# Kernel tuning notes

Measured on AMD Instinct MI355X. Metric: run time of the kernel, lower is better.

Reference implementation:

```python
import jax, jax.numpy as jnp
import numpy as np

N_HEAD = 16
DROP_P = 0.1


def setup_inputs() -> dict:
    key = jax.random.key(0)
    ks = jax.random.split(key, 5)
    B, T, C = 2, 2048, 1024
    return {
        "x": jax.random.normal(ks[0], (B, T, C), dtype=jnp.float32),
        "w_attn": jax.random.normal(ks[1], (C, 3 * C), dtype=jnp.float32) * 0.02,
        "b_attn": jax.random.normal(ks[2], (3 * C,), dtype=jnp.float32) * 0.02,
        "w_proj": jax.random.normal(ks[3], (C, C), dtype=jnp.float32) * 0.02,
        "b_proj": jax.random.normal(ks[4], (C,), dtype=jnp.float32) * 0.02,
    }


def reference(x, w_attn, b_attn, w_proj, b_proj):
    B, T, C = x.shape
    H = N_HEAD
    D = C // H  # head dim
    qkv = x @ w_attn + b_attn                      # [B,T,3C]
    q, k, v = jnp.split(qkv, 3, axis=-1)
    # [B,T,C] -> [B,H,T,D]
    q = q.reshape(B, T, H, D).transpose(0, 2, 1, 3)
    k = k.reshape(B, T, H, D).transpose(0, 2, 1, 3)
    v = v.reshape(B, T, H, D).transpose(0, 2, 1, 3)
    scale = 1.0 / jnp.sqrt(jnp.float32(D))
    attn = jnp.einsum("bhqd,bhkd->bhqk", q, k) * scale  # [B,H,T,T]
    causal = jnp.tril(jnp.ones((T, T), dtype=bool))
    attn = jnp.where(causal[None, None], attn, jnp.float32(-jnp.inf))
    attn = jax.nn.softmax(attn, axis=-1)
    # dropout p=0.1 (training mode in original); deterministic fixed key here
    keep = jax.random.bernoulli(jax.random.key(42), 1.0 - DROP_P, attn.shape)
    attn = jnp.where(keep, attn / (1.0 - DROP_P), 0.0)
    out = jnp.einsum("bhqk,bhkd->bhqd", attn, v)   # [B,H,T,D]
    out = out.transpose(0, 2, 1, 3).reshape(B, T, C)
    return out @ w_proj + b_proj
```

## Files before the change

### kernel.cpp

```cpp
#include <hip/hip_runtime.h>
#include <hip/hip_bf16.h>
#include <stdint.h>
#include <math.h>

#define TSEQ   2048
#define NBATCH 2
#define NHEAD  16
#define HDIM   64
#define CDIM   1024

#define KEEP_LIMIT 3865470464u
#define QSC 0.18033688011112042f

typedef short  bf16x8 __attribute__((ext_vector_type(8)));
typedef float  f32x4  __attribute__((ext_vector_type(4)));

__device__ __forceinline__ float fast_exp2(float x) {
    float r; asm("v_exp_f32 %0, %1" : "=v"(r) : "v"(x)); return r;
}
__device__ __forceinline__ uint32_t cvt_pk_bf16(float a, float b) {
    uint32_t r; asm("v_cvt_pk_bf16_f32 %0, %1, %2" : "=v"(r) : "v"(a), "v"(b)); return r;
}

__device__ __forceinline__ uint32_t rotl32(uint32_t x, int r) {
    return __builtin_amdgcn_alignbit(x, x, 32 - r);
}

__device__ __forceinline__ uint32_t tf2x32_xor(uint32_t x0, uint32_t x1) {
    const uint32_t ka = 0u, kb = 42u;
    const uint32_t kc = ka ^ kb ^ 0x1BD11BDAu;
    x0 += ka; x1 += kb;
#define TFR(r) { x0 += x1; x1 = rotl32(x1, r); x1 ^= x0; }
    TFR(13) TFR(15) TFR(26) TFR(6)
    x0 += kb; x1 += kc + 1u;
    TFR(17) TFR(29) TFR(16) TFR(24)
    x0 += kc; x1 += ka + 2u;
    TFR(13) TFR(15) TFR(26) TFR(6)
    x0 += ka; x1 += kb + 3u;
    TFR(17) TFR(29) TFR(16) TFR(24)
    x0 += kb; x1 += kc + 4u;
    TFR(13) TFR(15) TFR(26) TFR(6)
    x0 += kc; x1 += ka + 5u;
#undef TFR
    return x0 ^ x1;
}

__device__ __forceinline__ float bf2f(ushort u) {
    union { uint32_t i; float f; } c; c.i = ((uint32_t)u) << 16; return c.f;
}

__device__ __forceinline__ void async_copy16(void* lds, const void* g) {
    __builtin_amdgcn_global_load_lds(
        (const __attribute__((address_space(1))) unsigned int*)g,
        (__attribute__((address_space(3))) unsigned int*)lds, 16, 0, 0);
}

__global__ __launch_bounds__(256) void gen_mask(unsigned long long* __restrict__ mask)
{
    const int lane = threadIdx.x & 63;
    const int wv   = threadIdx.x >> 6;
    const int pair = blockIdx.x;
    const int hb   = blockIdx.y;
    const int half = blockIdx.z;
    for (int pass = 0; pass < 2; ++pass) {
        const int qt = pass ? 31 - pair : pair;
        const int nk = qt + 1;
        const int h0 = half ? (nk + 1) >> 1 : 0;
        const int h1 = half ? nk : (nk + 1) >> 1;
        const int ntask = (h1 - h0) << 6;
        const uint32_t qbase = ((uint32_t)hb << 11) + (uint32_t)(qt << 6);
        for (int t = wv; t < ntask; t += 4) {
            const int q  = t & 63;
            const int kt = h0 + (t >> 6);
            const uint32_t idx = (qbase + (uint32_t)q) * 2048u + (uint32_t)(kt << 6) + (uint32_t)lane;
            const bool keep = tf2x32_xor(0u, idx) < KEEP_LIMIT;
            const unsigned long long bal = __ballot(keep);
            if (lane == 0)
                mask[((size_t)(qbase + (uint32_t)q) << 5) + kt] = bal;
        }
    }
}

__global__ __launch_bounds__(256) void cvt_bf16(
    const float* __restrict__ src, ushort* __restrict__ dst, int n)
{
    int idx = (blockIdx.x * 256 + threadIdx.x) * 8;
    if (idx >= n) return;
    float4 a = *(const float4*)(src + idx);
    float4 b = *(const float4*)(src + idx + 4);
    uint4 o;
    o.x = cvt_pk_bf16(a.x, a.y); o.y = cvt_pk_bf16(a.z, a.w);
    o.z = cvt_pk_bf16(b.x, b.y); o.w = cvt_pk_bf16(b.z, b.w);
    *(uint4*)(dst + idx) = o;
}

__global__ __launch_bounds__(256) void transpose_cvt(
    const float* __restrict__ src, ushort* __restrict__ dst, int K, int N)
{
    __shared__ float t[32][33];
    const int n0 = blockIdx.x * 32, k0 = blockIdx.y * 32;
    const int i = threadIdx.x;
    {
        int k = i >> 3, n4 = (i & 7) * 4;
        float4 v = *(const float4*)(src + (size_t)(k0 + k) * N + n0 + n4);
        t[k][n4 + 0] = v.x; t[k][n4 + 1] = v.y; t[k][n4 + 2] = v.z; t[k][n4 + 3] = v.w;
    }
    __syncthreads();
    {
        int n = i >> 3, k4 = (i & 7) * 4;
        uint2 o;
        o.x = cvt_pk_bf16(t[k4 + 0][n], t[k4 + 1][n]);
        o.y = cvt_pk_bf16(t[k4 + 2][n], t[k4 + 3][n]);
        *(uint2*)(dst + (size_t)(n0 + n) * K + k0 + k4) = o;
    }
}

template<int MODE>
__global__ __launch_bounds__(256) void gemm_bf16(
    const ushort* __restrict__ A, const ushort* __restrict__ Bt,
    const float* __restrict__ bias,
    ushort* __restrict__ Q, ushort* __restrict__ Kq, ushort* __restrict__ V,
    float* __restrict__ Cf, int M, int N, int K)
{
    __shared__ ushort As[2][128 * 32];
    __shared__ ushort Bs[2][128 * 32];
    const int tid = threadIdx.x, lane = tid & 63, wid = tid >> 6;
    const int l15 = lane & 15, l4 = lane >> 4;
    const int wr = wid >> 1, wc = wid & 1;
    const int bn = blockIdx.x, bm = blockIdx.y;
    const int NTK = K >> 5;

    f32x4 acc[4][4];
#pragma unroll
    for (int m = 0; m < 4; ++m)
#pragma unroll
        for (int n = 0; n < 4; ++n) acc[m][n] = (f32x4){0.f, 0.f, 0.f, 0.f};

    auto stage = [&](int p, int k0) {
#pragma unroll
        for (int j = 0; j < 2; ++j) {
            const int rbase = wid * 32 + j * 16;
            const int row = rbase + (lane >> 2);
            const ushort* src = A + (size_t)(bm * 128 + row) * K + k0 + (lane & 3) * 8;
            async_copy16(&As[p][rbase * 32], src);
        }
#pragma unroll
        for (int j = 0; j < 2; ++j) {
            const int rbase = wid * 32 + j * 16;
            const int row = rbase + (lane >> 2);
            const ushort* src = Bt + (size_t)(bn * 128 + row) * K + k0 + (lane & 3) * 8;
            async_copy16(&Bs[p][rbase * 32], src);
        }
    };
    auto compute = [&](int p) {
        bf16x8 af[4], bf[4];
#pragma unroll
        for (int m = 0; m < 4; ++m)
            af[m] = *(const bf16x8*)&As[p][(wr * 64 + m * 16 + l15) * 32 + l4 * 8];
#pragma unroll
        for (int n = 0; n < 4; ++n)
            bf[n] = *(const bf16x8*)&Bs[p][(wc * 64 + n * 16 + l15) * 32 + l4 * 8];
#pragma unroll
        for (int m = 0; m < 4; ++m)
#pragma unroll
            for (int n = 0; n < 4; ++n)
                acc[m][n] = __builtin_amdgcn_mfma_f32_16x16x32_bf16(af[m], bf[n], acc[m][n], 0, 0, 0);
    };

    stage(0, 0);
    __syncthreads();
    for (int t = 0; t < NTK; ++t) {
        const int p = t & 1;
        if (t + 1 < NTK) stage(p ^ 1, (t + 1) << 5);
        compute(p);
        __syncthreads();
    }

    const int colbase = bn * 128 + wc * 64;
    const int rowbase = bm * 128 + wr * 64;
    if (MODE == 0) {
#pragma unroll
        for (int n = 0; n < 4; ++n) {
            const int col = colbase + n * 16 + l15;
            const float bv = bias[col];
#pragma unroll
            for (int m = 0; m < 4; ++m)
#pragma unroll
                for (int r = 0; r < 4; ++r) {
                    const int row = rowbase + m * 16 + l4 * 4 + r;
                    Cf[(size_t)row * N + col] = acc[m][n][r] + bv;
                }
        }
    } else {
#pragma unroll
        for (int n = 0; n < 4; ++n) {
            const int col = colbase + n * 16 + l15;
            const int which = col >> 10, cc = col & 1023;
            const int hh = cc >> 6, dd = cc & 63;
            const float bv = bias[col];
            const float sc = (which == 0) ? QSC : 1.0f;
#pragma unroll
            for (int m = 0; m < 4; ++m) {
                float v0 = (acc[m][n][0] + bv) * sc, v1 = (acc[m][n][1] + bv) * sc;
                float v2 = (acc[m][n][2] + bv) * sc, v3 = (acc[m][n][3] + bv) * sc;
                uint32_t pk01 = cvt_pk_bf16(v0, v1), pk23 = cvt_pk_bf16(v2, v3);
                ushort vals[4] = { (ushort)pk01, (ushort)(pk01 >> 16),
                                   (ushort)pk23, (ushort)(pk23 >> 16) };
#pragma unroll
                for (int r = 0; r < 4; ++r) {
                    const int row = rowbase + m * 16 + l4 * 4 + r;
                    const int bb = row >> 11, tt = row & 2047;
                    if (which == 0)
                        Q[(((size_t)(bb * NHEAD + hh)) * TSEQ + tt) * HDIM + dd] = vals[r];
                    else if (which == 1)
                        Kq[(((size_t)(bb * NHEAD + hh)) * TSEQ + tt) * HDIM + dd] = vals[r];
                    else
                        V[(((size_t)(bb * NHEAD + hh)) * HDIM + dd) * TSEQ + tt] = vals[r];
                }
            }
        }
    }
}

__global__ __launch_bounds__(256) void attn_fwd_mfma(
    const ushort* __restrict__ Qb, const ushort* __restrict__ Kb,
    const ushort* __restrict__ VbT, const unsigned long long* __restrict__ Mk,
    ushort* __restrict__ Ap, float* __restrict__ lp)
{
    __shared__ ushort Ks[64 * 64];
    __shared__ ushort Vt[2][64 * 64];
    __shared__ ushort Ps[64 * 64];
    const int tid = threadIdx.x;
    const int lane = tid & 63;
    const int wid = tid >> 6;
    const int l15 = lane & 15, l4 = lane >> 4;
    const int pair = blockIdx.x >> 1, half = blockIdx.x & 1;
    const int h = blockIdx.y, b = blockIdx.z;
    const int hb = b * NHEAD + h;
    const size_t headoff = (size_t)hb * TSEQ * HDIM;
    const ushort* Qg = Qb + headoff;
    const ushort* Kg = Kb + headoff;
    const ushort* Vg = VbT + headoff;

    auto stageK = [&](int kt) {
        const ushort* Kt = Kg + (size_t)(kt * 64) * HDIM;
#pragma unroll
        for (int c = 0; c < 2; ++c) {
            const int rbase = wid * 16 + c * 8;
            const int row = rbase + (lane >> 3);
            const ushort* srcK = Kt + row * 64 + (((lane & 7) * 8) ^ ((row & 7) << 3));
            async_copy16(&Ks[rbase * 64], srcK);
        }
    };
    auto stageV = [&](int p, int kt) {
        const ushort* Vt0 = Vg + kt * 64;
#pragma unroll
        for (int c = 0; c < 2; ++c) {
            const int rbase = wid * 16 + c * 8;
            const int row = rbase + (lane >> 3);
            const ushort* srcV = Vt0 + (size_t)row * TSEQ + (((lane & 7) * 8) ^ ((row & 7) << 3));
            async_copy16(&Vt[p][rbase * 64], srcV);
        }
    };

    const int swq = (l15 & 7) << 3;
    const int prow = wid * 16 + l15;

    for (int pass = 0; pass < 2; ++pass) {
        const int qt = pass ? (TSEQ / 64 - 1) - pair : pair;
        const int ntk = qt + 1;
        const int kb = half ? (ntk + 1) >> 1 : 0;
        const int ke = half ? ntk : (ntk + 1) >> 1;
        const int pidx = (hb * 32 + qt) * 2 + half;
        const int tilerow = wid * 16 + l15;
        ushort* arow = Ap + (size_t)pidx * 4096 + tilerow * 64;

        if (kb >= ke) {
#pragma unroll
            for (int dt = 0; dt < 4; ++dt) {
                ushort4 z; z.x = z.y = z.z = z.w = 0;
                *(ushort4*)&arow[dt * 16 + l4 * 4] = z;
            }
            if (l4 == 0) lp[pidx * 64 + tilerow] = 0.f;
            continue;
        }

        const int qglob = qt * 64 + tilerow;
        const unsigned long long* mrow = Mk + ((size_t)(hb * TSEQ + qglob) << 5);
        bf16x8 qf0, qf1;
        {
            const ushort* qrow = Qg + (size_t)qglob * HDIM;
            qf0 = *(const bf16x8*)(qrow + l4 * 8);
            qf1 = *(const bf16x8*)(qrow + 32 + l4 * 8);
        }

        f32x4 oacc[4];
#pragma unroll
        for (int i = 0; i < 4; ++i) oacc[i] = (f32x4){0.f, 0.f, 0.f, 0.f};
        float li = 0.f;

        stageK(kb);
        stageV(0, kb);
        __syncthreads();

        for (int kt = kb; kt < ke; ++kt) {
            const int p = (kt - kb) & 1;
            const bool hasNext = (kt + 1 < ke);
            if (hasNext) stageV(p ^ 1, kt + 1);

            const unsigned long long m64 = mrow[kt];

            f32x4 s4[4];
#pragma unroll
            for (int ct = 0; ct < 4; ++ct) {
                const int krow = ct * 16 + l15;
                const int sw = (krow & 7) << 3;
                bf16x8 kf0 = *(const bf16x8*)&Ks[krow * 64 + ((l4 * 8) ^ sw)];
                bf16x8 kf1 = *(const bf16x8*)&Ks[krow * 64 + ((l4 * 8 + 32) ^ sw)];
                f32x4 a = {0.f, 0.f, 0.f, 0.f};
                a = __builtin_amdgcn_mfma_f32_16x16x32_bf16(kf0, qf0, a, 0, 0, 0);
                a = __builtin_amdgcn_mfma_f32_16x16x32_bf16(kf1, qf1, a, 0, 0, 0);
                s4[ct] = a;
            }
            __syncthreads();
            if (hasNext) stageK(kt + 1);

            const int kb0 = kt * 64;
            if (kt == qt) {
#pragma unroll
                for (int ct = 0; ct < 4; ++ct)
#pragma unroll
                    for (int r = 0; r < 4; ++r) {
                        const int kglob = kb0 + ct * 16 + l4 * 4 + r;
                        s4[ct][r] = (kglob <= qglob) ? s4[ct][r] : -INFINITY;
                    }
            }
            float rs = 0.f;
#pragma unroll
            for (int ct = 0; ct < 4; ++ct)
#pragma unroll
                for (int r = 0; r < 4; ++r) {
                    s4[ct][r] = fast_exp2(s4[ct][r]);
                    rs += s4[ct][r];
                }
            li += rs;

#pragma unroll
            for (int ct = 0; ct < 4; ++ct) {
                const uint32_t nib = (uint32_t)(m64 >> (ct * 16 + l4 * 4)) & 0xFu;
                const float p0 = (nib & 1u) ? s4[ct][0] : 0.f;
                const float p1 = (nib & 2u) ? s4[ct][1] : 0.f;
                const float p2 = (nib & 4u) ? s4[ct][2] : 0.f;
                const float p3 = (nib & 8u) ? s4[ct][3] : 0.f;
                uint2 pk;
                pk.x = cvt_pk_bf16(p0, p1);
                pk.y = cvt_pk_bf16(p2, p3);
                *(uint2*)&Ps[prow * 64 + ((ct * 16 + l4 * 4) ^ swq)] = pk;
            }

            bf16x8 pf0 = *(const bf16x8*)&Ps[prow * 64 + ((l4 * 8) ^ swq)];
            bf16x8 pf1 = *(const bf16x8*)&Ps[prow * 64 + ((l4 * 8 + 32) ^ swq)];
#pragma unroll
            for (int dt = 0; dt < 4; ++dt) {
                const int drow = dt * 16 + l15;
                const int swv = (drow & 7) << 3;
                bf16x8 vf0 = *(const bf16x8*)&Vt[p][drow * 64 + ((l4 * 8) ^ swv)];
                bf16x8 vf1 = *(const bf16x8*)&Vt[p][drow * 64 + ((l4 * 8 + 32) ^ swv)];
                oacc[dt] = __builtin_amdgcn_mfma_f32_16x16x32_bf16(vf0, pf0, oacc[dt], 0, 0, 0);
                oacc[dt] = __builtin_amdgcn_mfma_f32_16x16x32_bf16(vf1, pf1, oacc[dt], 0, 0, 0);
            }
            __syncthreads();
        }

#pragma unroll
        for (int dt = 0; dt < 4; ++dt) {
            uint2 o;
            o.x = cvt_pk_bf16(oacc[dt][0], oacc[dt][1]);
            o.y = cvt_pk_bf16(oacc[dt][2], oacc[dt][3]);
            *(uint2*)&arow[dt * 16 + l4 * 4] = o;
        }
        float rs = li;
        rs += __shfl_xor(rs, 16);
        rs += __shfl_xor(rs, 32);
        if (l4 == 0) lp[pidx * 64 + tilerow] = rs;
    }
}

__global__ __launch_bounds__(256) void attn_merge(
    const ushort* __restrict__ Ap, const float* __restrict__ lp,
    ushort* __restrict__ AO)
{
    const int gidx = blockIdx.x * 16 + (threadIdx.x >> 4);
    const int hb = gidx >> 11;
    const int q  = gidx & 2047;
    const int qt = q >> 6, row = q & 63;
    const int sub = (threadIdx.x & 15) * 4;
    const int pidx0 = (hb * 32 + qt) * 2;
    const int pr = pidx0 * 64 + row;
    const float l0 = lp[pr], l1 = lp[pr + 64];
    const float inv = 1.0f / ((l0 + l1) * 0.9f);
    ushort4 a0 = *(const ushort4*)&Ap[(size_t)pidx0 * 4096 + row * 64 + sub];
    ushort4 a1 = *(const ushort4*)&Ap[(size_t)(pidx0 + 1) * 4096 + row * 64 + sub];
    const int b = hb >> 4, h = hb & 15;
    ushort* orow = AO + ((size_t)(b * TSEQ + q)) * CDIM + h * HDIM + sub;
    uint2 o;
    o.x = cvt_pk_bf16((bf2f(a0.x) + bf2f(a1.x)) * inv,
                      (bf2f(a0.y) + bf2f(a1.y)) * inv);
    o.y = cvt_pk_bf16((bf2f(a0.z) + bf2f(a1.z)) * inv,
                      (bf2f(a0.w) + bf2f(a1.w)) * inv);
    *(uint2*)orow = o;
}

extern "C" void kernel_launch(void* const* d_in, const int* in_sizes, int n_in,
                              void* d_out, int out_size, void* d_ws, size_t ws_size,
                              hipStream_t stream)
{
    const float* x      = (const float*)d_in[0];
    const float* w_attn = (const float*)d_in[1];
    const float* b_attn = (const float*)d_in[2];
    const float* w_proj = (const float*)d_in[3];
    const float* b_proj = (const float*)d_in[4];
    float* out = (float*)d_out;

    const size_t NH = (size_t)NBATCH * NHEAD * TSEQ * HDIM;
    ushort* Qb  = (ushort*)d_ws;
    ushort* Kb  = Qb + NH;
    ushort* VbT = Kb + NH;
    ushort* AO  = VbT + NH;
    ushort* xb  = AO + NH;
    ushort* wTa = xb + NH;
    ushort* wTp = wTa + (size_t)3072 * 1024;
    unsigned long long* Mk = (unsigned long long*)(wTp + (size_t)1024 * 1024);
    float*  lp  = (float*)(Mk + (size_t)65536 * 32);

    ushort* Aparts = (ushort*)d_out;

    cvt_bf16<<<2048, 256, 0, stream>>>(x, xb, 4096 * 1024);
    transpose_cvt<<<dim3(96, 32), 256, 0, stream>>>(w_attn, wTa, 1024, 3072);
    transpose_cvt<<<dim3(32, 32), 256, 0, stream>>>(w_proj, wTp, 1024, 1024);

    gemm_bf16<1><<<dim3(24, 32), 256, 0, stream>>>(
        xb, wTa, b_attn, Qb, Kb, VbT, nullptr, 4096, 3072, 1024);

    gen_mask<<<dim3(16, 32, 2), 256, 0, stream>>>(Mk);

    attn_fwd_mfma<<<dim3(32, NHEAD, NBATCH), 256, 0, stream>>>(
        Qb, Kb, VbT, Mk, Aparts, lp);

    attn_merge<<<4096, 256, 0, stream>>>(Aparts, lp, AO);

    gemm_bf16<0><<<dim3(8, 32), 256, 0, stream>>>(
        AO, wTp, b_proj, nullptr, nullptr, nullptr, out, 4096, 1024, 1024);
}
```

Measured before the change: 278.6 us.

## Merge prep kernels and co-schedule dropout mask generation with QKV GEMM

Folds the x conversion and both weight transposes into one prep launch. Merges dropout mask generation into the QKV GEMM launch as extra blocks, so the threefry hashing runs on CUs left idle by the 768 GEMM tiles. The mask blocks also get a new work split with four hashes in flight per wave. This cuts launch overhead and overlaps ALU-bound mask work with the MFMA-bound GEMM, at the cost of a more complex dispatch with heterogeneous blocks in one grid.

New measurement: 268.8 us. 3.5% less time.

```diff
diff --git a/kernel.cpp b/kernel.cpp
--- a/kernel.cpp
+++ b/kernel.cpp
@@ -55,51 +55,32 @@
         (__attribute__((address_space(3))) unsigned int*)lds, 16, 0, 0);
 }
 
-__global__ __launch_bounds__(256) void gen_mask(unsigned long long* __restrict__ mask)
-{
-    const int lane = threadIdx.x & 63;
-    const int wv   = threadIdx.x >> 6;
-    const int pair = blockIdx.x;
-    const int hb   = blockIdx.y;
-    const int half = blockIdx.z;
-    for (int pass = 0; pass < 2; ++pass) {
-        const int qt = pass ? 31 - pair : pair;
-        const int nk = qt + 1;
-        const int h0 = half ? (nk + 1) >> 1 : 0;
-        const int h1 = half ? nk : (nk + 1) >> 1;
-        const int ntask = (h1 - h0) << 6;
-        const uint32_t qbase = ((uint32_t)hb << 11) + (uint32_t)(qt << 6);
-        for (int t = wv; t < ntask; t += 4) {
-            const int q  = t & 63;
-            const int kt = h0 + (t >> 6);
-            const uint32_t idx = (qbase + (uint32_t)q) * 2048u + (uint32_t)(kt << 6) + (uint32_t)lane;
-            const bool keep = tf2x32_xor(0u, idx) < KEEP_LIMIT;
-            const unsigned long long bal = __ballot(keep);
-            if (lane == 0)
-                mask[((size_t)(qbase + (uint32_t)q) << 5) + kt] = bal;
-        }
-    }
-}
-
-__global__ __launch_bounds__(256) void cvt_bf16(
-    const float* __restrict__ src, ushort* __restrict__ dst, int n)
-{
-    int idx = (blockIdx.x * 256 + threadIdx.x) * 8;
-    if (idx >= n) return;
-    float4 a = *(const float4*)(src + idx);
-    float4 b = *(const float4*)(src + idx + 4);
-    uint4 o;
-    o.x = cvt_pk_bf16(a.x, a.y); o.y = cvt_pk_bf16(a.z, a.w);
-    o.z = cvt_pk_bf16(b.x, b.y); o.w = cvt_pk_bf16(b.z, b.w);
-    *(uint4*)(dst + idx) = o;
-}
-
-__global__ __launch_bounds__(256) void transpose_cvt(
-    const float* __restrict__ src, ushort* __restrict__ dst, int K, int N)
+__global__ __launch_bounds__(256) void prep(
+    const float* __restrict__ x, ushort* __restrict__ xb,
+    const float* __restrict__ wA, ushort* __restrict__ wTa,
+    const float* __restrict__ wP, ushort* __restrict__ wTp)
 {
     __shared__ float t[32][33];
-    const int n0 = blockIdx.x * 32, k0 = blockIdx.y * 32;
+    const int nb = blockIdx.x;
     const int i = threadIdx.x;
+    if (nb < 2048) {
+        int idx = (nb * 256 + i) * 8;
+        float4 a = *(const float4*)(x + idx);
+        float4 b = *(const float4*)(x + idx + 4);
+        uint4 o;
+        o.x = cvt_pk_bf16(a.x, a.y); o.y = cvt_pk_bf16(a.z, a.w);
+        o.z = cvt_pk_bf16(b.x, b.y); o.w = cvt_pk_bf16(b.z, b.w);
+        *(uint4*)(xb + idx) = o;
+        return;
+    }
+    const float* src; ushort* dst; int n0, k0, N, K;
+    if (nb < 5120) {
+        int tt = nb - 2048;  src = wA; dst = wTa;
+        n0 = (tt % 96) * 32; k0 = (tt / 96) * 32; N = 3072; K = 1024;
+    } else {
+        int tt = nb - 5120;  src = wP; dst = wTp;
+        n0 = (tt & 31) * 32; k0 = (tt >> 5) * 32; N = 1024; K = 1024;
+    }
     {
         int k = i >> 3, n4 = (i & 7) * 4;
         float4 v = *(const float4*)(src + (size_t)(k0 + k) * N + n0 + n4);
@@ -115,12 +96,136 @@
     }
 }
 
-template<int MODE>
-__global__ __launch_bounds__(256) void gemm_bf16(
+__global__ __launch_bounds__(256) void qkv_mask(
     const ushort* __restrict__ A, const ushort* __restrict__ Bt,
     const float* __restrict__ bias,
     ushort* __restrict__ Q, ushort* __restrict__ Kq, ushort* __restrict__ V,
-    float* __restrict__ Cf, int M, int N, int K)
+    unsigned long long* __restrict__ mask)
+{
+    __shared__ ushort As[2][128 * 32];
+    __shared__ ushort Bs[2][128 * 32];
+    const int tid = threadIdx.x, lane = tid & 63, wid = tid >> 6;
+
+    if (blockIdx.x >= 768) {
+        const int mb   = blockIdx.x - 768;
+        const int hb   = mb >> 6;
+        const int rem  = mb & 63;
+        const int pair = rem >> 2;
+        const int quad = rem & 3;
+        const int lim  = (pair + 1) << 6;
+        const int base = quad * 528 + wid * 132;
+#pragma unroll 1
+        for (int it = 0; it < 33; ++it) {
+            uint32_t idxs[4], qrow[4]; int kts[4];
+#pragma unroll
+            for (int j = 0; j < 4; ++j) {
+                const int u = base + it * 4 + j;
+                const bool first = (u < lim);
+                const int qt = first ? pair : 31 - pair;
+                const int uu = first ? u : u - lim;
+                const int kt = uu >> 6, q = uu & 63;
+                qrow[j] = ((uint32_t)hb << 11) + (uint32_t)((qt << 6) + q);
+                idxs[j] = qrow[j] * 2048u + (uint32_t)(kt << 6) + (uint32_t)lane;
+                kts[j] = kt;
+            }
+            uint32_t bits[4];
+#pragma unroll
+            for (int j = 0; j < 4; ++j) bits[j] = tf2x32_xor(0u, idxs[j]);
+#pragma unroll
+            for (int j = 0; j < 4; ++j) {
+                const unsigned long long bal = __ballot(bits[j] < KEEP_LIMIT);
+                if (lane == j)
+                    mask[((size_t)qrow[j] << 5) + kts[j]] = bal;
+            }
+        }
+        return;
+    }
+
+    const int l15 = lane & 15, l4 = lane >> 4;
+    const int wr = wid >> 1, wc = wid & 1;
+    const int bn = blockIdx.x % 24, bm = blockIdx.x / 24;
+    const int K = 1024, NTK = K >> 5;
+
+    f32x4 acc[4][4];
+#pragma unroll
+    for (int m = 0; m < 4; ++m)
+#pragma unroll
+        for (int n = 0; n < 4; ++n) acc[m][n] = (f32x4){0.f, 0.f, 0.f, 0.f};
+
+    auto stage = [&](int p, int k0) {
+#pragma unroll
+        for (int j = 0; j < 2; ++j) {
+            const int rbase = wid * 32 + j * 16;
+            const int row = rbase + (lane >> 2);
+            const ushort* src = A + (size_t)(bm * 128 + row) * K + k0 + (lane & 3) * 8;
+            async_copy16(&As[p][rbase * 32], src);
+        }
+#pragma unroll
+        for (int j = 0; j < 2; ++j) {
+            const int rbase = wid * 32 + j * 16;
+            const int row = rbase + (lane >> 2);
+            const ushort* src = Bt + (size_t)(bn * 128 + row) * K + k0 + (lane & 3) * 8;
+            async_copy16(&Bs[p][rbase * 32], src);
+        }
+    };
+    auto compute = [&](int p) {
+        bf16x8 af[4], bf[4];
+#pragma unroll
+        for (int m = 0; m < 4; ++m)
+            af[m] = *(const bf16x8*)&As[p][(wr * 64 + m * 16 + l15) * 32 + l4 * 8];
+#pragma unroll
+        for (int n = 0; n < 4; ++n)
+            bf[n] = *(const bf16x8*)&Bs[p][(wc * 64 + n * 16 + l15) * 32 + l4 * 8];
+#pragma unroll
+        for (int m = 0; m < 4; ++m)
+#pragma unroll
+            for (int n = 0; n < 4; ++n)
+                acc[m][n] = __builtin_amdgcn_mfma_f32_16x16x32_bf16(af[m], bf[n], acc[m][n], 0, 0, 0);
+    };
+
+    stage(0, 0);
+    __syncthreads();
+    for (int t = 0; t < NTK; ++t) {
+        const int p = t & 1;
+        if (t + 1 < NTK) stage(p ^ 1, (t + 1) << 5);
+        compute(p);
+        __syncthreads();
+    }
+
+    const int colbase = bn * 128 + wc * 64;
+    const int rowbase = bm * 128 + wr * 64;
+#pragma unroll
+    for (int n = 0; n < 4; ++n) {
+        const int col = colbase + n * 16 + l15;
+        const int which = col >> 10, cc = col & 1023;
+        const int hh = cc >> 6, dd = cc & 63;
+        const float bv = bias[col];
+        const float sc = (which == 0) ? QSC : 1.0f;
+#pragma unroll
+        for (int m = 0; m < 4; ++m) {
+            float v0 = (acc[m][n][0] + bv) * sc, v1 = (acc[m][n][1] + bv) * sc;
+            float v2 = (acc[m][n][2] + bv) * sc, v3 = (acc[m][n][3] + bv) * sc;
+            uint32_t pk01 = cvt_pk_bf16(v0, v1), pk23 = cvt_pk_bf16(v2, v3);
+            ushort vals[4] = { (ushort)pk01, (ushort)(pk01 >> 16),
+                               (ushort)pk23, (ushort)(pk23 >> 16) };
+#pragma unroll
+            for (int r = 0; r < 4; ++r) {
+                const int row = rowbase + m * 16 + l4 * 4 + r;
+                const int bb = row >> 11, tt = row & 2047;
+                if (which == 0)
+                    Q[(((size_t)(bb * NHEAD + hh)) * TSEQ + tt) * HDIM + dd] = vals[r];
+                else if (which == 1)
+                    Kq[(((size_t)(bb * NHEAD + hh)) * TSEQ + tt) * HDIM + dd] = vals[r];
+                else
+                    V[(((size_t)(bb * NHEAD + hh)) * HDIM + dd) * TSEQ + tt] = vals[r];
+            }
+        }
+    }
+}
+
+__global__ __launch_bounds__(256) void proj_gemm(
+    const ushort* __restrict__ A, const ushort* __restrict__ Bt,
+    const float* __restrict__ bias, float* __restrict__ Cf, int M, int N, int K)
 {
     __shared__ ushort As[2][128 * 32];
     __shared__ ushort Bs[2][128 * 32];
@@ -178,47 +283,17 @@
 
     const int colbase = bn * 128 + wc * 64;
     const int rowbase = bm * 128 + wr * 64;
-    if (MODE == 0) {
-#pragma unroll
-        for (int n = 0; n < 4; ++n) {
-            const int col = colbase + n * 16 + l15;
-            const float bv = bias[col];
-#pragma unroll
-            for (int m = 0; m < 4; ++m)
-#pragma unroll
-                for (int r = 0; r < 4; ++r) {
-                    const int row = rowbase + m * 16 + l4 * 4 + r;
-                    Cf[(size_t)row * N + col] = acc[m][n][r] + bv;
-                }
-        }
-    } else {
-#pragma unroll
-        for (int n = 0; n < 4; ++n) {
-            const int col = colbase + n * 16 + l15;
-            const int which = col >> 10, cc = col & 1023;
-            const int hh = cc >> 6, dd = cc & 63;
-            const float bv = bias[col];
-            const float sc = (which == 0) ? QSC : 1.0f;
-#pragma unroll
-            for (int m = 0; m < 4; ++m) {
-                float v0 = (acc[m][n][0] + bv) * sc, v1 = (acc[m][n][1] + bv) * sc;
-                float v2 = (acc[m][n][2] + bv) * sc, v3 = (acc[m][n][3] + bv) * sc;
-                uint32_t pk01 = cvt_pk_bf16(v0, v1), pk23 = cvt_pk_bf16(v2, v3);
-                ushort vals[4] = { (ushort)pk01, (ushort)(pk01 >> 16),
-                                   (ushort)pk23, (ushort)(pk23 >> 16) };
-#pragma unroll
-                for (int r = 0; r < 4; ++r) {
-                    const int row = rowbase + m * 16 + l4 * 4 + r;
-                    const int bb = row >> 11, tt = row & 2047;
-                    if (which == 0)
-                        Q[(((size_t)(bb * NHEAD + hh)) * TSEQ + tt) * HDIM + dd] = vals[r];
-                    else if (which == 1)
-                        Kq[(((size_t)(bb * NHEAD + hh)) * TSEQ + tt) * HDIM + dd] = vals[r];
-                    else
-                        V[(((size_t)(bb * NHEAD + hh)) * HDIM + dd) * TSEQ + tt] = vals[r];
-                }
-            }
-        }
+#pragma unroll
+    for (int n = 0; n < 4; ++n) {
+        const int col = colbase + n * 16 + l15;
+        const float bv = bias[col];
+#pragma unroll
+        for (int m = 0; m < 4; ++m)
+#pragma unroll
+            for (int r = 0; r < 4; ++r) {
+                const int row = rowbase + m * 16 + l4 * 4 + r;
+                Cf[(size_t)row * N + col] = acc[m][n][r] + bv;
+            }
     }
 }
 
@@ -435,20 +510,16 @@
 
     ushort* Aparts = (ushort*)d_out;
 
-    cvt_bf16<<<2048, 256, 0, stream>>>(x, xb, 4096 * 1024);
-    transpose_cvt<<<dim3(96, 32), 256, 0, stream>>>(w_attn, wTa, 1024, 3072);
-    transpose_cvt<<<dim3(32, 32), 256, 0, stream>>>(w_proj, wTp, 1024, 1024);
-
-    gemm_bf16<1><<<dim3(24, 32), 256, 0, stream>>>(
-        xb, wTa, b_attn, Qb, Kb, VbT, nullptr, 4096, 3072, 1024);
-
-    gen_mask<<<dim3(16, 32, 2), 256, 0, stream>>>(Mk);
+    prep<<<6144, 256, 0, stream>>>(x, xb, w_attn, wTa, w_proj, wTp);
+
+    qkv_mask<<<768 + 2048, 256, 0, stream>>>(
+        xb, wTa, b_attn, Qb, Kb, VbT, Mk);
 
     attn_fwd_mfma<<<dim3(32, NHEAD, NBATCH), 256, 0, stream>>>(
         Qb, Kb, VbT, Mk, Aparts, lp);
 
     attn_merge<<<4096, 256, 0, stream>>>(Aparts, lp, AO);
 
-    gemm_bf16<0><<<dim3(8, 32), 256, 0, stream>>>(
-        AO, wTp, b_proj, nullptr, nullptr, nullptr, out, 4096, 1024, 1024);
-}
+    proj_gemm<<<dim3(8, 32), 256, 0, stream>>>(
+        AO, wTp, b_proj, out, 4096, 1024, 1024);
+}
```
